# Optimization experiments

Hardware: AMD Instinct MI355X
Metric: run time of the kernel (lower is better)

Reference implementation:

```python
import jax, jax.numpy as jnp
import numpy as np


def _adj(M):
    # conjugate transpose of the last two (color) dims
    return jnp.conj(jnp.swapaxes(M, -1, -2))


def _plaquettes(U):
    # U: (B, L1..Ld, d, Nc, Nc) complex -> (B, L1..Ld, d*(d-1)/2, Nc, Nc)
    d = U.shape[-3]
    plaqs = []
    for mu in range(d):
        for nu in range(mu + 1, d):
            U_mu = U[..., mu, :, :]
            U_nu = U[..., nu, :, :]
            U_mu_fwd = jnp.roll(U_mu, -1, axis=1 + nu)
            U_nu_fwd = jnp.roll(U_nu, -1, axis=1 + mu)
            plaqs.append(U_mu @ U_nu_fwd @ _adj(U_mu_fwd) @ _adj(U_nu))
    return jnp.stack(plaqs, axis=-3)


def _polyakov(U):
    # Poly[..., mu] = U_mu(x) @ U_mu(x+mu) @ ... @ U_mu(x+(L_mu-1)mu)
    d = U.shape[-3]
    lattice_shape = U.shape[1:-3]
    loops = []
    for mu in range(d):
        U_mu = U[..., mu, :, :]
        P = U_mu
        shifted = U_mu
        for _ in range(1, lattice_shape[mu]):
            shifted = jnp.roll(shifted, -1, axis=1 + mu)
            P = P @ shifted
        loops.append(P)
    return jnp.stack(loops, axis=-3)


def setup_inputs() -> dict:
    key = jax.random.key(0)
    ks = jax.random.split(key, 4)
    B, L, d, Nc = 2, 16, 4, 3
    N_out, N_in, K = 8, 10, 1
    shapeU = (B, L, L, L, L, d, Nc, Nc)
    return {
        "U_re": jax.random.normal(ks[0], shapeU, jnp.float32),
        "U_im": jax.random.normal(ks[1], shapeU, jnp.float32),
        "omega_re": jax.random.normal(ks[2], (N_out, N_in, d, 2 * K + 1), jnp.float32),
        "omega_im": jax.random.normal(ks[3], (N_out, N_in, d, 2 * K + 1), jnp.float32),
        "K": K,
        "N_out": N_out,
    }


def reference(U_re, U_im, omega_re, omega_im, K, N_out):
    U = U_re + 1j * U_im            # complex64 gauge links (B, L1..L4, d, Nc, Nc)
    omega = omega_re + 1j * omega_im  # (N_out, N_in, d, 2K+1)
    d = U.shape[-3]

    # W = locally transforming variables: plaquettes + Polyakov loops, N_in channels
    W = jnp.concatenate([_plaquettes(U), _polyakov(U)], axis=-3)

    # NOTE: the original torch get_ParallelTransporters never writes the cumulative
    # products back into the tensor (in-place bug), so the transporters used by
    # L_conv are exactly U_mu for every shift k. We reproduce that behavior.
    W_conv = jnp.zeros(U.shape[:-3] + (N_out,) + U.shape[-2:], dtype=U.dtype)
    for k in range(-K, K + 1):
        i_k = k + K
        for mu in range(d):
            W_sh = jnp.roll(W, -k, axis=1 + mu)      # (B, lat, N_in, Nc, Nc)
            A = U[..., mu, :, :]                      # effective transporter (B, lat, Nc, Nc)
            W_conv = W_conv + jnp.einsum(
                'ij,...ac,...jcd,...db->...iab',
                omega[..., mu, i_k], A, W_sh, _adj(A), optimize=True)
    return W_conv
```

## Files before the change

### kernel.cpp

```cpp
#include <hip/hip_runtime.h>

#define LSZ   16
#define NBATCH 2
#define NSITE (NBATCH*LSZ*LSZ*LSZ*LSZ)
#define NIN   10
#define NOUT  8
#define ND    4
#define NCPLX ((long)NSITE * NOUT * 9)
#define NLINE_PER_DIR (NSITE / LSZ)
#define NLINK (NSITE * ND)
#define WSTRIDE 108

typedef unsigned int u32;
typedef float  f32x4 __attribute__((ext_vector_type(4)));
typedef short  s16x8 __attribute__((ext_vector_type(8)));

struct M3 { float re[9]; float im[9]; };

__device__ __forceinline__ unsigned short f2bf(float x) {
    u32 u = __float_as_uint(x);
    u32 r = (u + 0x7fffu + ((u >> 16) & 1u)) >> 16;
    return (unsigned short)r;
}
__device__ __forceinline__ u32 packbf(float lo, float hi) {
    return (u32)f2bf(lo) | ((u32)f2bf(hi) << 16);
}

__device__ __forceinline__ s16x8 as_s16x8(uint4 v) {
    union { uint4 u; s16x8 s; } x; x.u = v; return x.s;
}

__device__ __forceinline__ void mulM(M3& o, const M3& a, const M3& b) {
#pragma unroll
    for (int r = 0; r < 3; r++) {
#pragma unroll
        for (int c = 0; c < 3; c++) {
            float xr = 0.f, xi = 0.f;
#pragma unroll
            for (int k = 0; k < 3; k++) {
                float ar = a.re[r*3+k], ai = a.im[r*3+k];
                float br = b.re[k*3+c], bi = b.im[k*3+c];
                xr = fmaf(ar, br, xr); xr = fmaf(-ai, bi, xr);
                xi = fmaf(ar, bi, xi); xi = fmaf(ai, br, xi);
            }
            o.re[r*3+c] = xr; o.im[r*3+c] = xi;
        }
    }
}

__device__ __forceinline__ void mulAdjM(M3& o, const M3& a, const M3& b) {
#pragma unroll
    for (int r = 0; r < 3; r++) {
#pragma unroll
        for (int c = 0; c < 3; c++) {
            float xr = 0.f, xi = 0.f;
#pragma unroll
            for (int k = 0; k < 3; k++) {
                float ar = a.re[r*3+k], ai = a.im[r*3+k];
                float br = b.re[c*3+k], bi = b.im[c*3+k];
                xr = fmaf(ar, br, xr); xr = fmaf(ai, bi, xr);
                xi = fmaf(ai, br, xi); xi = fmaf(-ar, bi, xi);
            }
            o.re[r*3+c] = xr; o.im[r*3+c] = xi;
        }
    }
}

__device__ __forceinline__ int shift_site(int s, int mu, int k) {
    int sh = 12 - 4 * mu;
    int c  = (s >> sh) & 15;
    int nc = (c + k) & 15;
    return (s & ~(15 << sh)) | (nc << sh);
}

__global__ __launch_bounds__(256) void poly_kernel(const float* __restrict__ Ure,
                                                   const float* __restrict__ Uim,
                                                   u32* __restrict__ T2) {
    int lane = threadIdx.x & 63;
    int c    = lane & 15;
    int l    = lane >> 4;
    int wv   = threadIdx.x >> 6;
    int lineG = blockIdx.x * 16 + wv * 4 + l;
    int mu   = lineG / NLINE_PER_DIR;
    int lidx = lineG - mu * NLINE_PER_DIR;
    int sh   = 12 - 4 * mu;
    int low  = lidx & ((1 << sh) - 1);
    int high = lidx >> sh;
    int site = (high << (sh + 4)) | (c << sh) | low;
    long base = ((long)site * 4 + mu) * 9;

    M3 P;
#pragma unroll
    for (int e = 0; e < 9; e++) { P.re[e] = Ure[base + e]; P.im[e] = Uim[base + e]; }

#pragma unroll
    for (int k = 1; k < 16; k <<= 1) {
        int src = (lane & 48) | ((c + k) & 15);
        M3 Q, T;
#pragma unroll
        for (int e = 0; e < 9; e++) {
            Q.re[e] = __shfl(P.re[e], src);
            Q.im[e] = __shfl(P.im[e], src);
        }
        mulM(T, P, Q);
        P = T;
    }

    u32* Tp = T2 + base;
#pragma unroll
    for (int e = 0; e < 9; e++) Tp[e] = packbf(P.re[e], P.im[e]);
}

__global__ __launch_bounds__(192) void plaq_merge_kernel(const float* __restrict__ Ure,
                                                         const float* __restrict__ Uim,
                                                         const u32* __restrict__ T2,
                                                         u32* __restrict__ W) {
    __shared__ __align__(16) char smem[4 * 32 * 37 * sizeof(float2)];
    float2* sU = (float2*)smem;
    u32*    sw = (u32*)smem;

    int s0 = blockIdx.x * 32;

    u32 tpre[6]; int tofs[6];
#pragma unroll
    for (int w = 0; w < 6; w++) {
        int it = threadIdx.x + w * 192;
        tpre[w] = T2[(long)s0 * 36 + it];
        int ls2 = it / 36;
        int r   = it - ls2 * 36;
        int mu2 = r / 9;
        int e2  = r - mu2 * 9;
        tofs[w] = ls2 * WSTRIDE + e2 * 12 + 6 + mu2;
    }

    for (int n = threadIdx.x; n < 8 * 16 * 36; n += 192) {
        int run = n / 576;
        int q   = n - run * 576;
        int sir = q / 36;
        int e36 = q - sir * 36;
        int slot = run >> 1, r = run & 1;
        int base = s0 + r * 16;
        if (slot < 3) base = shift_site(base, slot, 1);
        long g = (long)(base + sir) * 36 + e36;
        sU[(slot * 32 + r * 16 + sir) * 37 + e36] = make_float2(Ure[g], Uim[g]);
    }
    __syncthreads();

    int p  = threadIdx.x >> 5;
    int ls = threadIdx.x & 31;

    int mu = (p < 3) ? 0 : ((p < 5) ? 1 : 2);
    int nu = (mu == 0) ? (p + 1) : ((mu == 1) ? (p - 1) : 3);

    M3 Umu, Unu, Unu_f, Umu_f, T1, T2m, P;
    {
        const float2* pp;
#define LDM(m, slot, site, link) \
        pp = &sU[((slot) * 32 + (site)) * 37 + (link) * 9]; \
        _Pragma("unroll") \
        for (int e = 0; e < 9; e++) { float2 v = pp[e]; (m).re[e] = v.x; (m).im[e] = v.y; }

        LDM(Umu, 3, ls, mu);
        LDM(Unu, 3, ls, nu);
        LDM(Unu_f, mu, ls, nu);
        int lsrot = (ls & 16) | ((ls + 1) & 15);
        int fslot = (nu == 3) ? 3 : nu;
        int fsite = (nu == 3) ? lsrot : ls;
        LDM(Umu_f, fslot, fsite, mu);
#undef LDM
    }

    mulM(T1, Umu, Unu_f);
    mulAdjM(T2m, T1, Umu_f);
    mulAdjM(P, T2m, Unu);

    __syncthreads();

#pragma unroll
    for (int e = 0; e < 9; e++) sw[ls * WSTRIDE + e * 12 + p] = packbf(P.re[e], P.im[e]);

    for (int it = threadIdx.x; it < 32 * 9 * 2; it += 192) {
        int site = it / 18;
        int r    = it - site * 18;
        sw[site * WSTRIDE + (r >> 1) * 12 + 10 + (r & 1)] = 0u;
    }

#pragma unroll
    for (int w = 0; w < 6; w++) sw[tofs[w]] = tpre[w];
    __syncthreads();

    uint4* W4 = (uint4*)W;
    for (int it = threadIdx.x; it < 27 * 32; it += 192) {
        int pl  = it >> 5;
        int ls2 = it & 31;
        int e   = pl / 3, q = pl - e * 3;
        const uint4 v = *(const uint4*)(sw + ls2 * WSTRIDE + e * 12 + q * 4);
        W4[(long)pl * NSITE + s0 + ls2] = v;
    }
}

template <int MODE>
__global__ __launch_bounds__(256) void conv_kernel(const float* __restrict__ Ure,
                                                   const float* __restrict__ Uim,
                                                   const u32* __restrict__ W,
                                                   const float* __restrict__ omre,
                                                   const float* __restrict__ omim,
                                                   float* __restrict__ out) {
    __shared__ __align__(16) char smraw[64 * 72 * sizeof(float)];
    uint4* somB = (uint4*)smraw;
    float* sout = (float*)smraw;

    for (int n = threadIdx.x; n < 12 * 64; n += 256) {
        int mk = n >> 6, ln = n & 63;
        int q = ln >> 4, c = ln & 15, i = c & 7;
        int mu = mk / 3, kk = mk - mu * 3;
        u32 wv[4];
#pragma unroll
        for (int w = 0; w < 4; w++) {
            int j = q * 4 + w;
            u32 val = 0u;
            if (q < 3 && j < NIN) {
                int oidx = ((i * NIN + j) * ND + mu) * 3 + kk;
                float orv = omre[oidx], oiv = omim[oidx];
                val = (c < 8) ? packbf(orv, -oiv) : packbf(oiv, orv);
            }
            wv[w] = val;
        }
        somB[n] = make_uint4(wv[0], wv[1], wv[2], wv[3]);
    }
    __syncthreads();

    int chunk = gridDim.x >> 3;
    int lb    = ((int)blockIdx.x & 7) * chunk + ((int)blockIdx.x >> 3);

    int lane = threadIdx.x & 63;
    int wv_  = threadIdx.x >> 6;
    int r    = lane & 15;
    int q    = lane >> 4;
    int s0b  = lb * 64;
    int sline = s0b + wv_ * 16;

    const uint4* W4 = (const uint4*)W;

    bool hi = (r >= 8);
    int  i  = r & 7;
    int  reg0 = hi ? 2 : 0;

    float accr[2][9], acci[2][9];
#pragma unroll
    for (int rr = 0; rr < 2; rr++)
#pragma unroll
        for (int e = 0; e < 9; e++) { accr[rr][e] = 0.f; acci[rr][e] = 0.f; }

    for (int mu = 0; mu < ND; mu++) {
        f32x4 acc[9];
#pragma unroll
        for (int e = 0; e < 9; e++) acc[e] = (f32x4)(0.f);

        for (int kk = 0; kk < 3; kk++) {
            int mk = mu * 3 + kk;
            s16x8 bfrag = as_s16x8(somB[mk * 64 + lane]);

            int nb;
            if (mu < 3) nb = shift_site(sline, mu, kk - 1) + r;
            else        nb = sline + ((r + kk - 1) & 15);

            uint4 w9[9];
            if (q < 3) {
#pragma unroll
                for (int e = 0; e < 9; e++) w9[e] = W4[(long)(e * 3 + q) * NSITE + nb];
            } else {
#pragma unroll
                for (int e = 0; e < 9; e++) w9[e] = make_uint4(0u, 0u, 0u, 0u);
            }
#pragma unroll
            for (int e = 0; e < 9; e++)
                acc[e] = __builtin_amdgcn_mfma_f32_16x16x32_bf16(as_s16x8(w9[e]), bfrag, acc[e], 0, 0, 0);
        }

        float own[2][9], oth[2][9];
#pragma unroll
        for (int e = 0; e < 9; e++) {
            float t0 = __shfl_xor(acc[e][0], 8);
            float t1 = __shfl_xor(acc[e][1], 8);
            float t2 = __shfl_xor(acc[e][2], 8);
            float t3 = __shfl_xor(acc[e][3], 8);
            own[0][e] = hi ? acc[e][2] : acc[e][0];
            own[1][e] = hi ? acc[e][3] : acc[e][1];
            oth[0][e] = hi ? t2 : t0;
            oth[1][e] = hi ? t3 : t1;
        }

#pragma unroll
        for (int rr = 0; rr < 2; rr++) {
            int site = sline + q * 4 + reg0 + rr;
            M3 A, M;
            {
                const float* pr = Ure + ((long)site * 4 + mu) * 9;
                const float* pi = Uim + ((long)site * 4 + mu) * 9;
#pragma unroll
                for (int e = 0; e < 9; e++) { A.re[e] = pr[e]; A.im[e] = pi[e]; }
            }
#pragma unroll
            for (int e = 0; e < 9; e++) {
                M.re[e] = hi ? oth[rr][e] : own[rr][e];
                M.im[e] = hi ? own[rr][e] : oth[rr][e];
            }
            M3 Tm;
#pragma unroll
            for (int rw = 0; rw < 3; rw++) {
#pragma unroll
                for (int cl = 0; cl < 3; cl++) {
                    float xr = 0.f, xi = 0.f;
#pragma unroll
                    for (int k = 0; k < 3; k++) {
                        float ar = A.re[rw*3+k], ai = A.im[rw*3+k];
                        float br = M.re[k*3+cl], bi = M.im[k*3+cl];
                        xr = fmaf(ar, br, xr); xr = fmaf(-ai, bi, xr);
                        xi = fmaf(ar, bi, xi); xi = fmaf(ai, br, xi);
                    }
                    Tm.re[rw*3+cl] = xr; Tm.im[rw*3+cl] = xi;
                }
            }
#pragma unroll
            for (int rw = 0; rw < 3; rw++) {
#pragma unroll
                for (int cl = 0; cl < 3; cl++) {
                    float xr = 0.f, xi = 0.f;
#pragma unroll
                    for (int k = 0; k < 3; k++) {
                        float ar = Tm.re[rw*3+k], ai = Tm.im[rw*3+k];
                        float br = A.re[cl*3+k], bi = A.im[cl*3+k];
                        xr = fmaf(ar, br, xr); xr = fmaf(ai, bi, xr);
                        if (MODE != 2) { xi = fmaf(ai, br, xi); xi = fmaf(-ar, bi, xi); }
                    }
                    accr[rr][rw*3+cl] += xr;
                    if (MODE != 2) acci[rr][rw*3+cl] += xi;
                }
            }
        }
    }

    if (MODE == 2) {
        __syncthreads();
#pragma unroll
        for (int rr = 0; rr < 2; rr++) {
            int tloc = wv_ * 16 + q * 4 + reg0 + rr;
#pragma unroll
            for (int e = 0; e < 9; e++)
                sout[(tloc * 8 + i) * 9 + e] = accr[rr][e];
        }
        __syncthreads();
        long base = (long)lb * 4608;
        for (int n = threadIdx.x; n < 4608; n += 256) out[base + n] = sout[n];
    } else if (MODE == 0) {
#pragma unroll
        for (int rr = 0; rr < 2; rr++) {
            int site = sline + q * 4 + reg0 + rr;
            long cb = ((long)site * 8 + i) * 9;
            float2* op = (float2*)(out + cb * 2);
#pragma unroll
            for (int e = 0; e < 9; e++) op[e] = make_float2(accr[rr][e], acci[rr][e]);
        }
    } else {
#pragma unroll
        for (int rr = 0; rr < 2; rr++) {
            int site = sline + q * 4 + reg0 + rr;
            long cb = ((long)site * 8 + i) * 9;
#pragma unroll
            for (int e = 0; e < 9; e++) {
                out[cb + e]         = accr[rr][e];
                out[NCPLX + cb + e] = acci[rr][e];
            }
        }
    }
}

extern "C" void kernel_launch(void* const* d_in, const int* in_sizes, int n_in,
                              void* d_out, int out_size, void* d_ws, size_t ws_size,
                              hipStream_t stream) {
    const float* Ure  = (const float*)d_in[0];
    const float* Uim  = (const float*)d_in[1];
    const float* omre = (const float*)d_in[2];
    const float* omim = (const float*)d_in[3];
    float* out = (float*)d_out;

    const size_t wBytes = (size_t)NSITE * WSTRIDE * sizeof(u32);
    if (ws_size < wBytes) return;

    u32* W  = (u32*)d_ws;
    u32* T2 = (u32*)d_out;

    poly_kernel<<<NSITE * 4 / (16 * 16), 256, 0, stream>>>(Ure, Uim, T2);
    plaq_merge_kernel<<<NSITE / 32, 192, 0, stream>>>(Ure, Uim, T2, W);

    const int convGrid = NSITE / 64;
    if (out_size == (int)NCPLX)
        conv_kernel<2><<<convGrid, 256, 0, stream>>>(Ure, Uim, W, omre, omim, out);
    else if (out_size == (int)(2 * NCPLX))
        conv_kernel<1><<<convGrid, 256, 0, stream>>>(Ure, Uim, W, omre, omim, out);
    else
        conv_kernel<0><<<convGrid, 256, 0, stream>>>(Ure, Uim, W, omre, omim, out);
}
```

Measured before the change: 239.8 us.

## Stage Polyakov links through LDS and load plaquette links directly from global

The Polyakov kernel now loads each block's 16 lines cooperatively into shared memory with a linear index pattern, then reads each thread's matrix from LDS. The goal is more coalesced global reads than the old per-thread strided loads. The plaquette kernel drops its shared-memory staging of the shifted link neighbourhoods and instead loads each 3x3 matrix straight from global with computed neighbour offsets. That removes a barrier and shrinks LDS use, at the cost of redundant, less coalesced global reads that now rely on the cache.

```diff
diff --git a/kernel.cpp b/kernel.cpp
--- a/kernel.cpp
+++ b/kernel.cpp
@@ -76,37 +76,57 @@
 __global__ __launch_bounds__(256) void poly_kernel(const float* __restrict__ Ure,
                                                    const float* __restrict__ Uim,
                                                    u32* __restrict__ T2) {
+    __shared__ float2 sm[16 * 145];
+
+    int line0 = blockIdx.x * 16;
+    int mu    = line0 / NLINE_PER_DIR;
+    int lidx0 = line0 - mu * NLINE_PER_DIR;
+    int sh    = 12 - 4 * mu;
+    int low0  = lidx0 & ((1 << sh) - 1);
+    int high0 = lidx0 >> sh;
+    int s_base0 = (high0 << (sh + 4)) | low0;
+
+    for (int n = threadIdx.x; n < 16 * 16 * 9; n += 256) {
+        int siteIdx = n / 9;
+        int e       = n - siteIdx * 9;
+        int site, l, c;
+        if (mu == 3) { site = (lidx0 << 4) + siteIdx; l = siteIdx >> 4; c = siteIdx & 15; }
+        else         { site = s_base0 + ((siteIdx >> 4) << sh) + (siteIdx & 15);
+                       l = siteIdx & 15; c = siteIdx >> 4; }
+        long g = ((long)site * 4 + mu) * 9 + e;
+        sm[l * 145 + c * 9 + e] = make_float2(Ure[g], Uim[g]);
+    }
+    __syncthreads();
+
     int lane = threadIdx.x & 63;
-    int c    = lane & 15;
-    int l    = lane >> 4;
-    int wv   = threadIdx.x >> 6;
-    int lineG = blockIdx.x * 16 + wv * 4 + l;
-    int mu   = lineG / NLINE_PER_DIR;
-    int lidx = lineG - mu * NLINE_PER_DIR;
-    int sh   = 12 - 4 * mu;
+    int c    = threadIdx.x & 15;
+    int l    = threadIdx.x >> 4;
+
+    M3 P;
+    {
+        const float2* m0 = &sm[l * 145 + c * 9];
+#pragma unroll
+        for (int e = 0; e < 9; e++) { float2 v = m0[e]; P.re[e] = v.x; P.im[e] = v.y; }
+    }
+
+#pragma unroll
+    for (int k = 1; k < 16; k <<= 1) {
+        int src = (lane & 48) | ((c + k) & 15);
+        M3 Q, T;
+#pragma unroll
+        for (int e = 0; e < 9; e++) {
+            Q.re[e] = __shfl(P.re[e], src);
+            Q.im[e] = __shfl(P.im[e], src);
+        }
+        mulM(T, P, Q);
+        P = T;
+    }
+
+    int lidx = lidx0 + l;
     int low  = lidx & ((1 << sh) - 1);
     int high = lidx >> sh;
     int site = (high << (sh + 4)) | (c << sh) | low;
-    long base = ((long)site * 4 + mu) * 9;
-
-    M3 P;
-#pragma unroll
-    for (int e = 0; e < 9; e++) { P.re[e] = Ure[base + e]; P.im[e] = Uim[base + e]; }
-
-#pragma unroll
-    for (int k = 1; k < 16; k <<= 1) {
-        int src = (lane & 48) | ((c + k) & 15);
-        M3 Q, T;
-#pragma unroll
-        for (int e = 0; e < 9; e++) {
-            Q.re[e] = __shfl(P.re[e], src);
-            Q.im[e] = __shfl(P.im[e], src);
-        }
-        mulM(T, P, Q);
-        P = T;
-    }
-
-    u32* Tp = T2 + base;
+    u32* Tp = T2 + ((long)site * 4 + mu) * 9;
 #pragma unroll
     for (int e = 0; e < 9; e++) Tp[e] = packbf(P.re[e], P.im[e]);
 }
@@ -115,9 +135,7 @@
                                                          const float* __restrict__ Uim,
                                                          const u32* __restrict__ T2,
                                                          u32* __restrict__ W) {
-    __shared__ __align__(16) char smem[4 * 32 * 37 * sizeof(float2)];
-    float2* sU = (float2*)smem;
-    u32*    sw = (u32*)smem;
+    __shared__ u32 sw[32 * WSTRIDE];
 
     int s0 = blockIdx.x * 32;
 
@@ -133,48 +151,28 @@
         tofs[w] = ls2 * WSTRIDE + e2 * 12 + 6 + mu2;
     }
 
-    for (int n = threadIdx.x; n < 8 * 16 * 36; n += 192) {
-        int run = n / 576;
-        int q   = n - run * 576;
-        int sir = q / 36;
-        int e36 = q - sir * 36;
-        int slot = run >> 1, r = run & 1;
-        int base = s0 + r * 16;
-        if (slot < 3) base = shift_site(base, slot, 1);
-        long g = (long)(base + sir) * 36 + e36;
-        sU[(slot * 32 + r * 16 + sir) * 37 + e36] = make_float2(Ure[g], Uim[g]);
-    }
-    __syncthreads();
-
     int p  = threadIdx.x >> 5;
     int ls = threadIdx.x & 31;
+    int s  = s0 + ls;
 
     int mu = (p < 3) ? 0 : ((p < 5) ? 1 : 2);
     int nu = (mu == 0) ? (p + 1) : ((mu == 1) ? (p - 1) : 3);
 
     M3 Umu, Unu, Unu_f, Umu_f, T1, T2m, P;
-    {
-        const float2* pp;
-#define LDM(m, slot, site, link) \
-        pp = &sU[((slot) * 32 + (site)) * 37 + (link) * 9]; \
+#define LDG(m, site, link) { \
+        long base_ = ((long)(site) * 4 + (link)) * 9; \
         _Pragma("unroll") \
-        for (int e = 0; e < 9; e++) { float2 v = pp[e]; (m).re[e] = v.x; (m).im[e] = v.y; }
-
-        LDM(Umu, 3, ls, mu);
-        LDM(Unu, 3, ls, nu);
-        LDM(Unu_f, mu, ls, nu);
-        int lsrot = (ls & 16) | ((ls + 1) & 15);
-        int fslot = (nu == 3) ? 3 : nu;
-        int fsite = (nu == 3) ? lsrot : ls;
-        LDM(Umu_f, fslot, fsite, mu);
-#undef LDM
-    }
+        for (int e = 0; e < 9; e++) { (m).re[e] = Ure[base_ + e]; (m).im[e] = Uim[base_ + e]; } }
+
+    LDG(Umu,   s,                      mu);
+    LDG(Unu,   s,                      nu);
+    LDG(Unu_f, shift_site(s, mu, 1),   nu);
+    LDG(Umu_f, shift_site(s, nu, 1),   mu);
+#undef LDG
 
     mulM(T1, Umu, Unu_f);
     mulAdjM(T2m, T1, Umu_f);
     mulAdjM(P, T2m, Unu);
-
-    __syncthreads();
 
 #pragma unroll
     for (int e = 0; e < 9; e++) sw[ls * WSTRIDE + e * 12 + p] = packbf(P.re[e], P.im[e]);
```

Result: faster. 220.1 us (-8.2%).
